# Optimization experiments

Hardware: AMD Instinct MI355X
Metric: run time of the kernel (lower is better)

Reference implementation:

```python
import jax, jax.numpy as jnp
import numpy as np

# ---- config (matches init_kwargs) ----
NUM_HEADS = 8
HEAD_DIM = 48
IN_CH = 384
OUT_CH = 384
AGENTS_HW = (7, 7)
CLUSTERS_HW = (2, 2)
NUM_MODULES = 2          # ['PartitionalClustering', 'FuzzyClustering']
N_GROUPS = 1 + 2 * NUM_MODULES   # p + (k, v) per module
D = NUM_HEADS * HEAD_DIM          # 384
NUM_CLUSTERS = CLUSTERS_HW[0] * CLUSTERS_HW[1]   # 4 per module
NUM_ALL_CLUSTERS = NUM_MODULES * NUM_CLUSTERS    # 8
EPS = 1e-6


def adaptive_avg_pool(x, oh, ow):
    # x: [b, c, H, W], H % oh == 0, W % ow == 0 -> exact block mean
    b, c, H, W = x.shape
    return x.reshape(b, c, oh, H // oh, ow, W // ow).mean(axis=(3, 5))


def setup_inputs() -> dict:
    key = jax.random.key(0)
    ks = jax.random.split(key, 6)
    B, H, W = 16, 56, 56
    x = jax.random.normal(ks[0], (B, IN_CH, H, W), dtype=jnp.float32)
    # proj: 1x1 linear in_channels -> N_GROUPS * D
    proj_w = jax.random.normal(ks[1], (N_GROUPS * D, IN_CH), dtype=jnp.float32) * (IN_CH ** -0.5)
    proj_b = jnp.zeros((N_GROUPS * D,), dtype=jnp.float32)
    sim_alpha = jnp.ones((NUM_ALL_CLUSTERS,), dtype=jnp.float32)
    sim_beta = jnp.zeros((NUM_ALL_CLUSTERS,), dtype=jnp.float32)
    proj2_w = jax.random.normal(ks[2], (OUT_CH, D), dtype=jnp.float32) * (D ** -0.5)
    proj2_b = jnp.zeros((OUT_CH,), dtype=jnp.float32)
    return {"x": x, "proj_w": proj_w, "proj_b": proj_b,
            "sim_alpha": sim_alpha, "sim_beta": sim_beta,
            "proj2_w": proj2_w, "proj2_b": proj2_b}


def _cluster_attention(i, k, v, kc, vc):
    # k: [b, c, Na] agent keys; v: [b, Na, c] agent values
    # kc, vc: [b, M, c] cluster centroids (keys / values)
    c = k.shape[1]
    scores = jnp.einsum('bmc,bcn->bmn', kc, k) / jnp.sqrt(jnp.float32(c))  # [b, M, Na]
    if i == 0:  # PartitionalClustering: attend over tokens per centroid
        attn = jax.nn.softmax(scores, axis=-1)
        agg = jnp.einsum('bmn,bnc->bmc', attn, v)
    else:       # FuzzyClustering: soft membership over clusters, normalized average
        memb = jax.nn.softmax(scores, axis=1)                              # over clusters
        agg = jnp.einsum('bmn,bnc->bmc', memb, v) / (memb.sum(axis=-1, keepdims=True) + EPS)
    return agg + vc  # with_cluster_bias=True


def reference(x, proj_w, proj_b, sim_alpha, sim_beta, proj2_w, proj2_b):
    B, C, H, W = x.shape
    # proj (1x1 linear over channels)
    y = jnp.einsum('bchw,oc->bohw', x, proj_w) + proj_b[None, :, None, None]
    y = y.reshape(B, N_GROUPS, D, H, W).transpose(1, 0, 2, 3, 4)
    b = B * NUM_HEADS
    c = HEAD_DIM
    y = y.reshape(N_GROUPS, b, c, H, W)
    p, r = y[0], y[1:]
    r = r.reshape(NUM_MODULES, 2, b, c, H, W)

    ah, aw = AGENTS_HW
    na = ah * aw
    agg_list = []
    for i in range(NUM_MODULES):  # fixed small structural loop
        k_full, v_full = r[i, 0], r[i, 1]
        kc = adaptive_avg_pool(k_full, *CLUSTERS_HW).reshape(b, c, NUM_CLUSTERS).transpose(0, 2, 1)
        vc = adaptive_avg_pool(v_full, *CLUSTERS_HW).reshape(b, c, NUM_CLUSTERS).transpose(0, 2, 1)
        k = adaptive_avg_pool(k_full, ah, aw).reshape(b, c, na)             # [b, c, Na]
        v = adaptive_avg_pool(v_full, ah, aw).reshape(b, c, na).transpose(0, 2, 1)  # [b, Na, c]
        agg_list.append(_cluster_attention(i, k, v, kc, vc))
    agg = jnp.concatenate(agg_list, axis=1)  # [b, M_all, c]

    p_agents = adaptive_avg_pool(p, ah, aw).reshape(b, c, na)  # [b, c, Na]
    # cosine similarity between centroid aggregates and query tokens
    agg_n = agg / (jnp.linalg.norm(agg, axis=-1, keepdims=True) + EPS)
    p_n = p_agents / (jnp.linalg.norm(p_agents, axis=1, keepdims=True) + EPS)
    sim = jnp.einsum('bmc,bcn->bmn', agg_n, p_n)  # [b, M_all, Na]
    similarity = sim_alpha[None, :, None] * sim + sim_beta[None, :, None]
    assignment = jax.nn.softmax(similarity, axis=1)  # over clusters

    out = jnp.einsum('bmc,bmn->bcn', agg, assignment)  # [b, c, Na]
    out = out.reshape(b, c, ah, aw)
    # bilinear upsample (half-pixel centers == torch align_corners=False)
    out = jax.image.resize(out, (b, c, H, W), method='linear')
    out = out.reshape(B, D, H, W)
    out = jnp.einsum('bdhw,od->bohw', out, proj2_w) + proj2_b[None, :, None, None]
    return out
```

## Files before the change

kernel.cpp:

```cpp
#include <hip/hip_runtime.h>
#include <math.h>

#define CIN    384
#define NPIX   3136

typedef float vf4 __attribute__((ext_vector_type(4)));
typedef __attribute__((ext_vector_type(4))) float f32x4;
typedef __attribute__((ext_vector_type(8))) short bf16x8;
typedef __attribute__((ext_vector_type(8))) unsigned short u16x8;

__device__ __forceinline__ unsigned short f2bf(float f) {
    unsigned u = __float_as_uint(f);
    u = (u + 0x7FFF + ((u >> 16) & 1)) >> 16;
    return (unsigned short)u;
}
__device__ __forceinline__ float bf2f(unsigned short h) {
    return __uint_as_float(((unsigned)h) << 16);
}

__global__ __launch_bounds__(256) void k_front(const float* __restrict__ x,
                                               const float* __restrict__ W1,
                                               const float* __restrict__ W2,
                                               unsigned short* __restrict__ Xhi,
                                               unsigned short* __restrict__ Xlo,
                                               unsigned short* __restrict__ Whi1,
                                               unsigned short* __restrict__ Wlo1,
                                               unsigned short* __restrict__ Whi2,
                                               unsigned short* __restrict__ Wlo2) {
    int blk = blockIdx.x;
    int t = threadIdx.x;
    if (blk >= 9024) {
        int i = (blk - 9024) * 256 + t;
        float w = W2[i];
        unsigned short hi = f2bf(w);
        Whi2[i] = hi;
        Wlo2[i] = f2bf(w - bf2f(hi));
        return;
    }
    if (blk >= 6144) {
        int i = (blk - 6144) * 256 + t;
        float w = W1[i];
        unsigned short hi = f2bf(w);
        Whi1[i] = hi;
        Wlo1[i] = f2bf(w - bf2f(hi));
        return;
    }
    int Bi = blk / CIN;
    int ch = blk - Bi * CIN;
    __shared__ float ps[56][14];
    __shared__ float s14[14][14];
    const float* xp = x + (size_t)(Bi * CIN + ch) * NPIX;
    for (int p = t; p < 784; p += 256) {
        int row = p / 14, cb = p % 14;
        const vf4 v = __builtin_nontemporal_load(
            reinterpret_cast<const vf4*>(xp + row * 56 + cb * 4));
        ps[row][cb] = v.x + v.y + v.z + v.w;
    }
    __syncthreads();
    if (t < 196) {
        int ri = t / 14, cb = t % 14;
        s14[ri][cb] = ps[4*ri][cb] + ps[4*ri+1][cb] + ps[4*ri+2][cb] + ps[4*ri+3][cb];
    }
    __syncthreads();
    if (t < 49) {
        int i = t / 7, j = t % 7;
        float s = (s14[2*i][2*j] + s14[2*i][2*j+1] + s14[2*i+1][2*j] + s14[2*i+1][2*j+1])
                  * (1.0f / 64.0f);
        int p = Bi * 49 + t;
        unsigned short hi = f2bf(s);
        Xhi[(size_t)p * 384 + ch] = hi;
        Xlo[(size_t)p * 384 + ch] = f2bf(s - bf2f(hi));
    } else if (t >= 64 && t < 68) {
        int m = t - 64;
        int mi = m / 2, mj = m % 2;
        float s = 0.f;
        for (int ri = 7*mi; ri < 7*mi + 7; ++ri)
            for (int cb = 7*mj; cb < 7*mj + 7; ++cb)
                s += s14[ri][cb];
        s *= (1.0f / 784.0f);
        int p = 784 + Bi * 4 + m;
        unsigned short hi = f2bf(s);
        Xhi[(size_t)p * 384 + ch] = hi;
        Xlo[(size_t)p * 384 + ch] = f2bf(s - bf2f(hi));
    }
}

__global__ __launch_bounds__(512) void k_fuse(
        const unsigned short* __restrict__ Whi, const unsigned short* __restrict__ Wlo,
        const unsigned short* __restrict__ Xhi, const unsigned short* __restrict__ Xlo,
        const float* __restrict__ proj_b,
        const float* __restrict__ alpha, const float* __restrict__ beta,
        unsigned short* __restrict__ osThi, unsigned short* __restrict__ osTlo) {
    int bb = blockIdx.x;
    int Bi = bb >> 3, head = bb & 7;
    __shared__ float yT[16560];
    __shared__ float e0[4][49], memb[4][49];
    __shared__ float rowmax0[4], esum0[4], msum[4];
    __shared__ float agg[8][48];
    __shared__ float anorm[8], pnorm[49];
    __shared__ float simL[8][49];
    __shared__ float assignW[8][49];
    unsigned short* sAh = (unsigned short*)yT;
    unsigned short* sAl = sAh + 9600;
    unsigned short* sBh = sAl + 9600;
    unsigned short* sBl = sBh + 2560;
    int t = threadIdx.x;
    int lane = t & 63, w = t >> 6;
    int fr = lane & 15, fq = lane >> 4;

    int row0 = t >> 2, ko0 = (t & 3) * 8;
    int g0 = row0 / 48, cc0 = row0 - g0 * 48;
    size_t aoff0 = (size_t)(g0 * 384 + head * 48 + cc0) * 384 + ko0;
    int c1 = t + 512;
    int row1 = c1 >> 2, ko1 = (c1 & 3) * 8;
    int g1 = row1 / 48, cc1 = row1 - g1 * 48;
    size_t aoff1 = (size_t)(g1 * 384 + head * 48 + cc1) * 384 + ko1;
    int bko = (t & 3) * 8;
    int brow = t >> 2;
    int bp = brow < 49 ? Bi * 49 + brow : 784 + Bi * 4 + (brow - 49);
    size_t boff = (size_t)bp * 384 + bko;

    u16x8 rAh0, rAl0, rAh1, rAl1, rBh, rBl;
    rAh0 = *(const u16x8*)(Whi + aoff0);
    rAl0 = *(const u16x8*)(Wlo + aoff0);
    if (t < 448) { rAh1 = *(const u16x8*)(Whi + aoff1); rAl1 = *(const u16x8*)(Wlo + aoff1); }
    if (t < 212) { rBh  = *(const u16x8*)(Xhi + boff);  rBl  = *(const u16x8*)(Xlo + boff); }

    f32x4 acc[2][4] = {};
    for (int step = 0; step < 12; ++step) {
        *(u16x8*)&sAh[row0 * 40 + ko0] = rAh0;
        *(u16x8*)&sAl[row0 * 40 + ko0] = rAl0;
        if (t < 448) {
            *(u16x8*)&sAh[row1 * 40 + ko1] = rAh1;
            *(u16x8*)&sAl[row1 * 40 + ko1] = rAl1;
        }
        if (t < 212) {
            *(u16x8*)&sBh[brow * 40 + bko] = rBh;
            *(u16x8*)&sBl[brow * 40 + bko] = rBl;
        }
        __syncthreads();
        if (step < 11) {
            int k0 = (step + 1) * 32;
            rAh0 = *(const u16x8*)(Whi + aoff0 + k0);
            rAl0 = *(const u16x8*)(Wlo + aoff0 + k0);
            if (t < 448) { rAh1 = *(const u16x8*)(Whi + aoff1 + k0); rAl1 = *(const u16x8*)(Wlo + aoff1 + k0); }
            if (t < 212) { rBh  = *(const u16x8*)(Xhi + boff + k0);  rBl  = *(const u16x8*)(Xlo + boff + k0); }
        }
        bf16x8 bh[4], bl[4];
#pragma unroll
        for (int nt = 0; nt < 4; ++nt) {
            int r = nt * 16 + fr;
            bh[nt] = *(const bf16x8*)&sBh[r * 40 + fq * 8];
            bl[nt] = *(const bf16x8*)&sBl[r * 40 + fq * 8];
        }
#pragma unroll
        for (int mi = 0; mi < 2; ++mi) {
            int mt = 2 * w + mi;
            if (mt < 15) {
                int r = mt * 16 + fr;
                bf16x8 ah = *(const bf16x8*)&sAh[r * 40 + fq * 8];
                bf16x8 al = *(const bf16x8*)&sAl[r * 40 + fq * 8];
#pragma unroll
                for (int nt = 0; nt < 4; ++nt) {
                    acc[mi][nt] = __builtin_amdgcn_mfma_f32_16x16x32_bf16(ah, bh[nt], acc[mi][nt], 0, 0, 0);
                    acc[mi][nt] = __builtin_amdgcn_mfma_f32_16x16x32_bf16(ah, bl[nt], acc[mi][nt], 0, 0, 0);
                    acc[mi][nt] = __builtin_amdgcn_mfma_f32_16x16x32_bf16(al, bh[nt], acc[mi][nt], 0, 0, 0);
                }
            }
        }
        __syncthreads();
    }
#pragma unroll
    for (int mi = 0; mi < 2; ++mi) {
        int mt = 2 * w + mi;
        if (mt < 15) {
#pragma unroll
            for (int j = 0; j < 4; ++j) {
                int m = mt * 16 + fq * 4 + j;
                int g = m / 48, cc = m - g * 48;
                float bb = proj_b[g * 384 + head * 48 + cc];
#pragma unroll
                for (int nt = 0; nt < 4; ++nt)
                    yT[m * 69 + nt * 16 + fr] = acc[mi][nt][j] + bb;
            }
        }
    }
    __syncthreads();

    const float scale = 0.14433756729740643f;
    if (t < 392) {
        int i = t / 196, r = t % 196;
        int m = r / 49, n = r % 49;
        int rbase = 48 + 96 * i;
        float s = 0.f;
        for (int cc = 0; cc < 48; ++cc)
            s += yT[(rbase + cc) * 69 + 49 + m] * yT[(rbase + cc) * 69 + n];
        s *= scale;
        if (i == 0) e0[m][n] = s; else memb[m][n] = s;
    }
    __syncthreads();
    if (t < 4) {
        float mx = -1e30f;
        for (int n = 0; n < 49; ++n) mx = fmaxf(mx, e0[t][n]);
        rowmax0[t] = mx;
    }
    __syncthreads();
    if (t < 196) { int m = t / 49, n = t % 49; e0[m][n] = expf(e0[m][n] - rowmax0[m]); }
    __syncthreads();
    if (t < 4) { float s = 0.f; for (int n = 0; n < 49; ++n) s += e0[t][n]; esum0[t] = s; }
    if (t >= 64 && t < 113) {
        int n = t - 64;
        float a0 = memb[0][n], a1 = memb[1][n], a2 = memb[2][n], a3 = memb[3][n];
        float mx = fmaxf(fmaxf(a0, a1), fmaxf(a2, a3));
        float x0 = expf(a0 - mx), x1 = expf(a1 - mx), x2 = expf(a2 - mx), x3 = expf(a3 - mx);
        float s = x0 + x1 + x2 + x3;
        memb[0][n] = x0 / s; memb[1][n] = x1 / s; memb[2][n] = x2 / s; memb[3][n] = x3 / s;
    }
    __syncthreads();
    if (t < 4) { float s = 0.f; for (int n = 0; n < 49; ++n) s += memb[t][n]; msum[t] = s; }
    __syncthreads();
    if (t < 384) {
        int row = t / 48, cc = t % 48;
        float a = 0.f;
        if (row < 4) {
            const float* vr = &yT[(96 + cc) * 69];
            for (int n = 0; n < 49; ++n) a += e0[row][n] * vr[n];
            agg[row][cc] = a / esum0[row] + vr[49 + row];
        } else {
            int m = row - 4;
            const float* vr = &yT[(192 + cc) * 69];
            for (int n = 0; n < 49; ++n) a += memb[m][n] * vr[n];
            agg[row][cc] = a / (msum[m] + 1e-6f) + vr[49 + m];
        }
    }
    __syncthreads();
    if (t < 8) {
        float s = 0.f;
        for (int cc = 0; cc < 48; ++cc) { float a = agg[t][cc]; s += a * a; }
        anorm[t] = sqrtf(s) + 1e-6f;
    }
    if (t >= 64 && t < 113) {
        int n = t - 64; float s = 0.f;
        for (int cc = 0; cc < 48; ++cc) { float a = yT[cc * 69 + n]; s += a * a; }
        pnorm[n] = sqrtf(s) + 1e-6f;
    }
    __syncthreads();
    if (t < 392) {
        int m = t / 49, n = t - m * 49;
        float dot = 0.f;
        for (int cc = 0; cc < 48; ++cc) dot += agg[m][cc] * yT[cc * 69 + n];
        simL[m][n] = alpha[m] * (dot / (anorm[m] * pnorm[n])) + beta[m];
    }
    __syncthreads();
    if (t < 49) {
        int n = t;
        float mx = -1e30f, e[8];
        for (int m = 0; m < 8; ++m) mx = fmaxf(mx, simL[m][n]);
        float ssum = 0.f;
        for (int m = 0; m < 8; ++m) { e[m] = expf(simL[m][n] - mx); ssum += e[m]; }
        float inv = 1.f / ssum;
        for (int m = 0; m < 8; ++m) assignW[m][n] = e[m] * inv;
    }
    __syncthreads();
    for (int idx = t; idx < 3072; idx += 512) {
        int n = idx / 48, cc = idx - n * 48;
        float s = 0.f;
        if (n < 49)
            for (int m = 0; m < 8; ++m) s += agg[m][cc] * assignW[m][n];
        size_t o = ((size_t)(Bi * 64 + n)) * 384 + head * 48 + cc;
        unsigned short hi = f2bf(s);
        osThi[o] = hi;
        osTlo[o] = f2bf(s - bf2f(hi));
    }
}

__global__ __launch_bounds__(512) void k_gemm2m(
        const unsigned short* __restrict__ Whi2, const unsigned short* __restrict__ Wlo2,
        const unsigned short* __restrict__ osThi, const unsigned short* __restrict__ osTlo,
        float* __restrict__ z) {
    int blk = blockIdx.x;
    int Bi = blk / 3, rg = blk - Bi * 3;
    __shared__ unsigned short sAh[128 * 40], sAl[128 * 40];
    __shared__ unsigned short sBh[64 * 40],  sBl[64 * 40];
    int t = threadIdx.x;
    int lane = t & 63, w = t >> 6;
    int fr = lane & 15, fq = lane >> 4;
    int arow = t >> 2, ako = (t & 3) * 8;
    size_t aoff = (size_t)(rg * 128 + arow) * 384 + ako;
    int brow = (t & 255) >> 2, bko = (t & 3) * 8;
    size_t boff = ((size_t)(Bi * 64 + brow)) * 384 + bko;
    f32x4 acc[4] = {};
    for (int k0 = 0; k0 < 384; k0 += 32) {
        *(u16x8*)&sAh[arow * 40 + ako] = *(const u16x8*)(Whi2 + aoff + k0);
        *(u16x8*)&sAl[arow * 40 + ako] = *(const u16x8*)(Wlo2 + aoff + k0);
        if (t < 256) {
            *(u16x8*)&sBh[brow * 40 + bko] = *(const u16x8*)(osThi + boff + k0);
            *(u16x8*)&sBl[brow * 40 + bko] = *(const u16x8*)(osTlo + boff + k0);
        }
        __syncthreads();
        int r = w * 16 + fr;
        bf16x8 ah = *(const bf16x8*)&sAh[r * 40 + fq * 8];
        bf16x8 al = *(const bf16x8*)&sAl[r * 40 + fq * 8];
#pragma unroll
        for (int nt = 0; nt < 4; ++nt) {
            int rb = nt * 16 + fr;
            bf16x8 bh = *(const bf16x8*)&sBh[rb * 40 + fq * 8];
            bf16x8 bl = *(const bf16x8*)&sBl[rb * 40 + fq * 8];
            acc[nt] = __builtin_amdgcn_mfma_f32_16x16x32_bf16(ah, bh, acc[nt], 0, 0, 0);
            acc[nt] = __builtin_amdgcn_mfma_f32_16x16x32_bf16(ah, bl, acc[nt], 0, 0, 0);
            acc[nt] = __builtin_amdgcn_mfma_f32_16x16x32_bf16(al, bh, acc[nt], 0, 0, 0);
        }
        __syncthreads();
    }
#pragma unroll
    for (int j = 0; j < 4; ++j) {
        int ch = rg * 128 + w * 16 + fq * 4 + j;
#pragma unroll
        for (int nt = 0; nt < 4; ++nt) {
            int col = nt * 16 + fr;
            if (col < 49)
                z[((size_t)(Bi * 384 + ch)) * 52 + col] = acc[nt][j];
        }
    }
}

__global__ __launch_bounds__(256) void k_up4(const float* __restrict__ z,
                                             const float* __restrict__ b2,
                                             float* __restrict__ out) {
    int blk = blockIdx.x;
    int Bi = blk / 96, cg = blk - Bi * 96;
    int ch0 = cg * 4;
    __shared__ float zL[4][52];
    __shared__ float tmp[4][56][8];
    int t = threadIdx.x;
    if (t < 196) {
        int c = t / 49, n = t - c * 49;
        zL[c][n] = z[((size_t)(Bi * 384 + ch0 + c)) * 52 + n] + b2[ch0 + c];
    }
    __syncthreads();
    for (int idx = t; idx < 1568; idx += 256) {
        int c = idx / 392, rem = idx - c * 392;
        int h = rem / 7, iw = rem - h * 7;
        float sh = (h - 3.5f) * 0.125f;
        int ih0; float fh;
        if (sh <= 0.f)      { ih0 = 0; fh = 0.f; }
        else if (sh >= 6.f) { ih0 = 6; fh = 0.f; }
        else                { ih0 = (int)sh; fh = sh - (float)ih0; }
        int ih1 = min(ih0 + 1, 6);
        float z0 = zL[c][ih0 * 7 + iw];
        tmp[c][h][iw] = z0 + fh * (zL[c][ih1 * 7 + iw] - z0);
    }
    __syncthreads();
    size_t obase = ((size_t)(Bi * 384 + ch0)) * (size_t)NPIX;
    for (int q = t; q < 3136; q += 256) {
        int c = q / 784, rem = q - c * 784;
        int h = rem / 14, qw = rem - h * 14;
        const float* tr = &tmp[c][h][0];
        vf4 o4;
#pragma unroll
        for (int j = 0; j < 4; ++j) {
            int w = qw * 4 + j;
            float sw = (w - 3.5f) * 0.125f;
            int iw0; float fw;
            if (sw <= 0.f)      { iw0 = 0; fw = 0.f; }
            else if (sw >= 6.f) { iw0 = 6; fw = 0.f; }
            else                { iw0 = (int)sw; fw = sw - (float)iw0; }
            int iw1 = min(iw0 + 1, 6);
            float t0 = tr[iw0];
            o4[j] = t0 + fw * (tr[iw1] - t0);
        }
        __builtin_nontemporal_store(o4,
            reinterpret_cast<vf4*>(out + obase + (size_t)q * 4));
    }
}

extern "C" void kernel_launch(void* const* d_in, const int* in_sizes, int n_in,
                              void* d_out, int out_size, void* d_ws, size_t ws_size,
                              hipStream_t stream) {
    const float* x      = (const float*)d_in[0];
    const float* proj_w = (const float*)d_in[1];
    const float* proj_b = (const float*)d_in[2];
    const float* alpha  = (const float*)d_in[3];
    const float* beta   = (const float*)d_in[4];
    const float* w2     = (const float*)d_in[5];
    const float* b2     = (const float*)d_in[6];
    float* out = (float*)d_out;
    float* ws  = (float*)d_ws;

    float* z = ws;
    unsigned short* Whi1  = (unsigned short*)(ws + (size_t)319488);
    unsigned short* Wlo1  = (unsigned short*)(ws + (size_t)688128);
    unsigned short* Xhi   = (unsigned short*)(ws + (size_t)1056768);
    unsigned short* Xlo   = (unsigned short*)(ws + (size_t)1228800);
    unsigned short* Whi2  = (unsigned short*)(ws + (size_t)1400832);
    unsigned short* Wlo2  = (unsigned short*)(ws + (size_t)1474560);
    unsigned short* osThi = (unsigned short*)(ws + (size_t)1548288);
    unsigned short* osTlo = (unsigned short*)(ws + (size_t)1744896);

    k_front <<<dim3(9600), 256, 0, stream>>>(x, proj_w, w2, Xhi, Xlo, Whi1, Wlo1, Whi2, Wlo2);
    k_fuse  <<<dim3(128),  512, 0, stream>>>(Whi1, Wlo1, Xhi, Xlo, proj_b, alpha, beta, osThi, osTlo);
    k_gemm2m<<<dim3(48),   512, 0, stream>>>(Whi2, Wlo2, osThi, osTlo, z);
    k_up4   <<<dim3(1536), 256, 0, stream>>>(z, b2, out);
}
```

Baseline: 74.36 us.

## Fuse second projection GEMM into upsample kernel and warp-shuffle softmax reductions

Merges the proj2 GEMM kernel and the bilinear upsample kernel into one tail kernel. Each block computes its 4 output channels via MFMA, keeps the results in shared memory, and upsamples directly, which removes the z round-trip through global memory and one launch. In k_fuse, the serial single-thread softmax and norm reductions are replaced with wavefront shuffle reductions and fast __expf. The cost is that each of the 1536 blocks reloads the full osT tile for its batch and wastes 12 of 16 MFMA rows on zero-padding.

```diff
diff --git a/kernel.cpp b/kernel.cpp
--- a/kernel.cpp
+++ b/kernel.cpp
@@ -95,7 +95,7 @@
     int Bi = bb >> 3, head = bb & 7;
     __shared__ float yT[16560];
     __shared__ float e0[4][49], memb[4][49];
-    __shared__ float rowmax0[4], esum0[4], msum[4];
+    __shared__ float msum[4];
     __shared__ float agg[8][48];
     __shared__ float anorm[8], pnorm[49];
     __shared__ float simL[8][49];
@@ -199,25 +199,33 @@
         if (i == 0) e0[m][n] = s; else memb[m][n] = s;
     }
     __syncthreads();
-    if (t < 4) {
-        float mx = -1e30f;
-        for (int n = 0; n < 49; ++n) mx = fmaxf(mx, e0[t][n]);
-        rowmax0[t] = mx;
-    }
-    __syncthreads();
-    if (t < 196) { int m = t / 49, n = t % 49; e0[m][n] = expf(e0[m][n] - rowmax0[m]); }
-    __syncthreads();
-    if (t < 4) { float s = 0.f; for (int n = 0; n < 49; ++n) s += e0[t][n]; esum0[t] = s; }
-    if (t >= 64 && t < 113) {
-        int n = t - 64;
+    if (w < 4) {
+        float v = (lane < 49) ? e0[w][lane] : -1e30f;
+        float mx = v;
+#pragma unroll
+        for (int off = 32; off; off >>= 1) mx = fmaxf(mx, __shfl_xor(mx, off));
+        float e = (lane < 49) ? __expf(v - mx) : 0.f;
+        float s = e;
+#pragma unroll
+        for (int off = 32; off; off >>= 1) s += __shfl_xor(s, off);
+        if (lane < 49) e0[w][lane] = e / s;
+    } else if (w == 4 && lane < 49) {
+        int n = lane;
         float a0 = memb[0][n], a1 = memb[1][n], a2 = memb[2][n], a3 = memb[3][n];
         float mx = fmaxf(fmaxf(a0, a1), fmaxf(a2, a3));
-        float x0 = expf(a0 - mx), x1 = expf(a1 - mx), x2 = expf(a2 - mx), x3 = expf(a3 - mx);
+        float x0 = __expf(a0 - mx), x1 = __expf(a1 - mx);
+        float x2 = __expf(a2 - mx), x3 = __expf(a3 - mx);
         float s = x0 + x1 + x2 + x3;
         memb[0][n] = x0 / s; memb[1][n] = x1 / s; memb[2][n] = x2 / s; memb[3][n] = x3 / s;
     }
     __syncthreads();
-    if (t < 4) { float s = 0.f; for (int n = 0; n < 49; ++n) s += memb[t][n]; msum[t] = s; }
+    if (w >= 4) {
+        int m = w - 4;
+        float v = (lane < 49) ? memb[m][lane] : 0.f;
+#pragma unroll
+        for (int off = 32; off; off >>= 1) v += __shfl_xor(v, off);
+        if (lane == 0) msum[m] = v;
+    }
     __syncthreads();
     if (t < 384) {
         int row = t / 48, cc = t % 48;
@@ -225,7 +233,7 @@
         if (row < 4) {
             const float* vr = &yT[(96 + cc) * 69];
             for (int n = 0; n < 49; ++n) a += e0[row][n] * vr[n];
-            agg[row][cc] = a / esum0[row] + vr[49 + row];
+            agg[row][cc] = a + vr[49 + row];
         } else {
             int m = row - 4;
             const float* vr = &yT[(192 + cc) * 69];
@@ -234,13 +242,15 @@
         }
     }
     __syncthreads();
-    if (t < 8) {
-        float s = 0.f;
-        for (int cc = 0; cc < 48; ++cc) { float a = agg[t][cc]; s += a * a; }
-        anorm[t] = sqrtf(s) + 1e-6f;
-    }
-    if (t >= 64 && t < 113) {
-        int n = t - 64; float s = 0.f;
+    {
+        float v = 0.f;
+        if (lane < 48) { float a = agg[w][lane]; v = a * a; }
+#pragma unroll
+        for (int off = 32; off; off >>= 1) v += __shfl_xor(v, off);
+        if (lane == 0) anorm[w] = sqrtf(v) + 1e-6f;
+    }
+    if (t < 49) {
+        int n = t; float s = 0.f;
         for (int cc = 0; cc < 48; ++cc) { float a = yT[cc * 69 + n]; s += a * a; }
         pnorm[n] = sqrtf(s) + 1e-6f;
     }
@@ -257,7 +267,7 @@
         float mx = -1e30f, e[8];
         for (int m = 0; m < 8; ++m) mx = fmaxf(mx, simL[m][n]);
         float ssum = 0.f;
-        for (int m = 0; m < 8; ++m) { e[m] = expf(simL[m][n] - mx); ssum += e[m]; }
+        for (int m = 0; m < 8; ++m) { e[m] = __expf(simL[m][n] - mx); ssum += e[m]; }
         float inv = 1.f / ssum;
         for (int m = 0; m < 8; ++m) assignW[m][n] = e[m] * inv;
     }
@@ -274,68 +284,51 @@
     }
 }
 
-__global__ __launch_bounds__(512) void k_gemm2m(
+__global__ __launch_bounds__(256) void k_tail(
         const unsigned short* __restrict__ Whi2, const unsigned short* __restrict__ Wlo2,
         const unsigned short* __restrict__ osThi, const unsigned short* __restrict__ osTlo,
-        float* __restrict__ z) {
+        const float* __restrict__ b2, float* __restrict__ out) {
     int blk = blockIdx.x;
-    int Bi = blk / 3, rg = blk - Bi * 3;
-    __shared__ unsigned short sAh[128 * 40], sAl[128 * 40];
-    __shared__ unsigned short sBh[64 * 40],  sBl[64 * 40];
+    int Bi = blk / 96, cg = blk - Bi * 96;
+    int ch0 = cg * 4;
+    __shared__ unsigned short sAh[16 * 40], sAl[16 * 40];
+    __shared__ unsigned short sBh[64 * 40], sBl[64 * 40];
+    __shared__ float zL[4][64];
+    __shared__ float tmp[4][56][8];
     int t = threadIdx.x;
     int lane = t & 63, w = t >> 6;
     int fr = lane & 15, fq = lane >> 4;
-    int arow = t >> 2, ako = (t & 3) * 8;
-    size_t aoff = (size_t)(rg * 128 + arow) * 384 + ako;
-    int brow = (t & 255) >> 2, bko = (t & 3) * 8;
+    for (int idx = t; idx < 480; idx += 256) {
+        int r = 4 + idx / 40, c = idx % 40;
+        sAh[r * 40 + c] = 0; sAl[r * 40 + c] = 0;
+    }
+    int brow = t >> 2, bko = (t & 3) * 8;
     size_t boff = ((size_t)(Bi * 64 + brow)) * 384 + bko;
-    f32x4 acc[4] = {};
+    f32x4 acc = {0, 0, 0, 0};
     for (int k0 = 0; k0 < 384; k0 += 32) {
-        *(u16x8*)&sAh[arow * 40 + ako] = *(const u16x8*)(Whi2 + aoff + k0);
-        *(u16x8*)&sAl[arow * 40 + ako] = *(const u16x8*)(Wlo2 + aoff + k0);
-        if (t < 256) {
-            *(u16x8*)&sBh[brow * 40 + bko] = *(const u16x8*)(osThi + boff + k0);
-            *(u16x8*)&sBl[brow * 40 + bko] = *(const u16x8*)(osTlo + boff + k0);
-        }
+        if (t < 16) {
+            int arow = t >> 2, ako = (t & 3) * 8;
+            size_t aoff = (size_t)(ch0 + arow) * 384 + k0 + ako;
+            *(u16x8*)&sAh[arow * 40 + ako] = *(const u16x8*)(Whi2 + aoff);
+            *(u16x8*)&sAl[arow * 40 + ako] = *(const u16x8*)(Wlo2 + aoff);
+        }
+        *(u16x8*)&sBh[brow * 40 + bko] = *(const u16x8*)(osThi + boff + k0);
+        *(u16x8*)&sBl[brow * 40 + bko] = *(const u16x8*)(osTlo + boff + k0);
         __syncthreads();
-        int r = w * 16 + fr;
-        bf16x8 ah = *(const bf16x8*)&sAh[r * 40 + fq * 8];
-        bf16x8 al = *(const bf16x8*)&sAl[r * 40 + fq * 8];
-#pragma unroll
-        for (int nt = 0; nt < 4; ++nt) {
-            int rb = nt * 16 + fr;
-            bf16x8 bh = *(const bf16x8*)&sBh[rb * 40 + fq * 8];
-            bf16x8 bl = *(const bf16x8*)&sBl[rb * 40 + fq * 8];
-            acc[nt] = __builtin_amdgcn_mfma_f32_16x16x32_bf16(ah, bh, acc[nt], 0, 0, 0);
-            acc[nt] = __builtin_amdgcn_mfma_f32_16x16x32_bf16(ah, bl, acc[nt], 0, 0, 0);
-            acc[nt] = __builtin_amdgcn_mfma_f32_16x16x32_bf16(al, bh, acc[nt], 0, 0, 0);
-        }
+        bf16x8 ah = *(const bf16x8*)&sAh[fr * 40 + fq * 8];
+        bf16x8 al = *(const bf16x8*)&sAl[fr * 40 + fq * 8];
+        int rb = w * 16 + fr;
+        bf16x8 bh = *(const bf16x8*)&sBh[rb * 40 + fq * 8];
+        bf16x8 bl = *(const bf16x8*)&sBl[rb * 40 + fq * 8];
+        acc = __builtin_amdgcn_mfma_f32_16x16x32_bf16(ah, bh, acc, 0, 0, 0);
+        acc = __builtin_amdgcn_mfma_f32_16x16x32_bf16(ah, bl, acc, 0, 0, 0);
+        acc = __builtin_amdgcn_mfma_f32_16x16x32_bf16(al, bh, acc, 0, 0, 0);
         __syncthreads();
     }
-#pragma unroll
-    for (int j = 0; j < 4; ++j) {
-        int ch = rg * 128 + w * 16 + fq * 4 + j;
-#pragma unroll
-        for (int nt = 0; nt < 4; ++nt) {
-            int col = nt * 16 + fr;
-            if (col < 49)
-                z[((size_t)(Bi * 384 + ch)) * 52 + col] = acc[nt][j];
-        }
-    }
-}
-
-__global__ __launch_bounds__(256) void k_up4(const float* __restrict__ z,
-                                             const float* __restrict__ b2,
-                                             float* __restrict__ out) {
-    int blk = blockIdx.x;
-    int Bi = blk / 96, cg = blk - Bi * 96;
-    int ch0 = cg * 4;
-    __shared__ float zL[4][52];
-    __shared__ float tmp[4][56][8];
-    int t = threadIdx.x;
-    if (t < 196) {
-        int c = t / 49, n = t - c * 49;
-        zL[c][n] = z[((size_t)(Bi * 384 + ch0 + c)) * 52 + n] + b2[ch0 + c];
+    if (fq == 0) {
+#pragma unroll
+        for (int j = 0; j < 4; ++j)
+            zL[j][w * 16 + fr] = acc[j] + b2[ch0 + j];
     }
     __syncthreads();
     for (int idx = t; idx < 1568; idx += 256) {
@@ -359,8 +352,8 @@
         vf4 o4;
 #pragma unroll
         for (int j = 0; j < 4; ++j) {
-            int w = qw * 4 + j;
-            float sw = (w - 3.5f) * 0.125f;
+            int ww = qw * 4 + j;
+            float sw = (ww - 3.5f) * 0.125f;
             int iw0; float fw;
             if (sw <= 0.f)      { iw0 = 0; fw = 0.f; }
             else if (sw >= 6.f) { iw0 = 6; fw = 0.f; }
@@ -387,18 +380,16 @@
     float* out = (float*)d_out;
     float* ws  = (float*)d_ws;
 
-    float* z = ws;
-    unsigned short* Whi1  = (unsigned short*)(ws + (size_t)319488);
-    unsigned short* Wlo1  = (unsigned short*)(ws + (size_t)688128);
-    unsigned short* Xhi   = (unsigned short*)(ws + (size_t)1056768);
-    unsigned short* Xlo   = (unsigned short*)(ws + (size_t)1228800);
-    unsigned short* Whi2  = (unsigned short*)(ws + (size_t)1400832);
-    unsigned short* Wlo2  = (unsigned short*)(ws + (size_t)1474560);
-    unsigned short* osThi = (unsigned short*)(ws + (size_t)1548288);
-    unsigned short* osTlo = (unsigned short*)(ws + (size_t)1744896);
-
-    k_front <<<dim3(9600), 256, 0, stream>>>(x, proj_w, w2, Xhi, Xlo, Whi1, Wlo1, Whi2, Wlo2);
-    k_fuse  <<<dim3(128),  512, 0, stream>>>(Whi1, Wlo1, Xhi, Xlo, proj_b, alpha, beta, osThi, osTlo);
-    k_gemm2m<<<dim3(48),   512, 0, stream>>>(Whi2, Wlo2, osThi, osTlo, z);
-    k_up4   <<<dim3(1536), 256, 0, stream>>>(z, b2, out);
-}
+    unsigned short* Whi1  = (unsigned short*)(ws);
+    unsigned short* Wlo1  = (unsigned short*)(ws + (size_t)368640);
+    unsigned short* Xhi   = (unsigned short*)(ws + (size_t)737280);
+    unsigned short* Xlo   = (unsigned short*)(ws + (size_t)909312);
+    unsigned short* Whi2  = (unsigned short*)(ws + (size_t)1081344);
+    unsigned short* Wlo2  = (unsigned short*)(ws + (size_t)1155072);
+    unsigned short* osThi = (unsigned short*)(ws + (size_t)1228800);
+    unsigned short* osTlo = (unsigned short*)(ws + (size_t)1425408);
+
+    k_front<<<dim3(9600), 256, 0, stream>>>(x, proj_w, w2, Xhi, Xlo, Whi1, Wlo1, Whi2, Wlo2);
+    k_fuse <<<dim3(128),  512, 0, stream>>>(Whi1, Wlo1, Xhi, Xlo, proj_b, alpha, beta, osThi, osTlo);
+    k_tail <<<dim3(1536), 256, 0, stream>>>(Whi2, Wlo2, osThi, osTlo, b2, out);
+}
```

New measurement: 73.04 us. Within noise of the previous version (-1.8%).
